# Kernel tuning notes

Measured on AMD Instinct MI355X. Metric: run time of the kernel, lower is better.

## Reference

```python
import jax, jax.numpy as jnp
import numpy as np
from jax import lax

B = 16384
NWIRES = 4


def _conv(x, w, b):
    # NCHW conv, stride 1, SAME padding (pad 1 for k=3)
    y = lax.conv_general_dilated(x, w, (1, 1), ((1, 1), (1, 1)),
                                 dimension_numbers=("NCHW", "OIHW", "NCHW"))
    return y + b[None, :, None, None]


def _pool2(x):
    b, c, h, w = x.shape
    return x.reshape(b, c, h // 2, 2, w // 2, 2).max(axis=(3, 5))


def _apply_1q(state, U, wire):
    # state: (B,2,2,2,2) complex; U: (B,2,2) complex
    s = jnp.moveaxis(state, wire + 1, -1)
    s = jnp.einsum("bij,b...j->b...i", U, s)
    return jnp.moveaxis(s, -1, wire + 1)


def _apply_cnot(state, c, t):
    s0 = jnp.take(state, 0, axis=c + 1)
    s1 = jnp.take(state, 1, axis=c + 1)
    ta = t + 1 if t < c else t  # target axis index after removing control axis
    s1 = jnp.flip(s1, axis=ta)
    return jnp.stack([s0, s1], axis=c + 1)


def _ry(th):
    c = jnp.cos(th / 2)
    s = jnp.sin(th / 2)
    U = jnp.stack([jnp.stack([c, -s], -1), jnp.stack([s, c], -1)], -2)
    return U.astype(jnp.complex64)


def _rz(th):
    e = jnp.exp(-0.5j * th.astype(jnp.complex64))
    z = jnp.zeros_like(e)
    return jnp.stack([jnp.stack([e, z], -1), jnp.stack([z, jnp.conj(e)], -1)], -2)


def _rx(th):
    c = jnp.cos(th / 2).astype(jnp.complex64)
    s = jnp.sin(th / 2).astype(jnp.complex64)
    return jnp.stack([jnp.stack([c, -1j * s], -1), jnp.stack([-1j * s, c], -1)], -2)


def _circuit(params):
    # params: (B, 16) -> PauliZ expvals (B, 4)
    b = params.shape[0]
    state = jnp.zeros((b, 16), jnp.complex64).at[:, 0].set(1.0).reshape(b, 2, 2, 2, 2)
    for i in range(NWIRES):
        state = _apply_1q(state, _ry(params[:, 4 * i + 0]), i)
        state = _apply_1q(state, _rz(params[:, 4 * i + 1]), i)
        state = _apply_1q(state, _rx(params[:, 4 * i + 2]), i)
        state = _apply_cnot(state, i, (i + 1) % NWIRES)
    probs = state.real ** 2 + state.imag ** 2  # (B,2,2,2,2)
    zs = []
    for i in range(NWIRES):
        p = probs.sum(axis=tuple(a for a in range(1, 5) if a != i + 1))  # (B,2)
        zs.append(p[:, 0] - p[:, 1])
    return jnp.stack(zs, axis=-1)


def setup_inputs() -> dict:
    key = jax.random.key(0)
    ks = jax.random.split(key, 12)
    d = {}
    d["x"] = jax.random.normal(ks[0], (B, 1, 28, 28), jnp.float32)
    d["conv1_w"] = jax.random.normal(ks[1], (4, 1, 3, 3), jnp.float32) * 0.3
    d["conv1_b"] = jax.random.normal(ks[2], (4,), jnp.float32) * 0.1
    d["conv2_w"] = jax.random.normal(ks[3], (4, 4, 3, 3), jnp.float32) * 0.15
    d["conv2_b"] = jax.random.normal(ks[4], (4,), jnp.float32) * 0.1
    d["pl_w"] = jax.random.normal(ks[5], (16, 196), jnp.float32) * 0.07
    d["pl_b"] = jax.random.normal(ks[6], (16,), jnp.float32) * 0.05
    d["ro_w"] = jax.random.normal(ks[7], (4, 4), jnp.float32) * 0.5
    d["ro_b"] = jax.random.normal(ks[8], (4,), jnp.float32) * 0.1
    d["bn_w"] = jnp.ones((4,), jnp.float32)
    d["bn_b"] = jnp.zeros((4,), jnp.float32)
    return d


def reference(x, conv1_w, conv1_b, conv2_w, conv2_b, pl_w, pl_b, ro_w, ro_b, bn_w, bn_b):
    h = _pool2(jax.nn.relu(_conv(x, conv1_w, conv1_b)))   # (B,4,14,14)
    h = _pool2(jax.nn.relu(_conv(h, conv2_w, conv2_b)))   # (B,4,7,7)
    flat = h.reshape(x.shape[0], -1)                      # (B,196)
    params = flat @ pl_w.T + pl_b                         # (B,16)
    z = _circuit(params)                                  # (B,4)
    out = z @ ro_w.T + ro_b                               # (B,4)
    mean = out.mean(0)
    var = out.var(0)  # biased, matches torch BN training normalization
    return (out - mean) / jnp.sqrt(var + 1e-5) * bn_w + bn_b
```

## Files before the change

### kernel.cpp

```cpp
#include <hip/hip_runtime.h>
#include <math.h>

#define BATCH 16384

typedef float v2f __attribute__((ext_vector_type(2)));
typedef unsigned short u16;
typedef __attribute__((ext_vector_type(8))) short short8;
typedef __attribute__((ext_vector_type(4))) float f32x4;

__device__ __forceinline__ v2f pk_fma(v2f a, v2f b, v2f c) {
  return __builtin_elementwise_fma(a, b, c);
}
__device__ __forceinline__ v2f pk_max(v2f a, v2f b) {
  return __builtin_elementwise_max(a, b);
}

__device__ __forceinline__ unsigned bf2(float lo, float hi) {
  unsigned a = __float_as_uint(lo);
  unsigned b = __float_as_uint(hi);
  a = (a + 0x7fffu + ((a >> 16) & 1u)) >> 16;
  b = (b + 0x7fffu + ((b >> 16) & 1u)) & 0xffff0000u;
  return a | b;
}

__device__ __forceinline__ unsigned cvtpk(float lo, float hi) {
  unsigned r;
  asm("v_cvt_pk_bf16_f32 %0, %1, %2" : "=v"(r) : "v"(lo), "v"(hi));
  return r;
}

__global__ __launch_bounds__(256) void qnat_fused(
    const float* __restrict__ x,
    const float* __restrict__ w1,
    const float* __restrict__ b1,
    const float* __restrict__ w2,
    const float* __restrict__ b2,
    const float* __restrict__ plw,
    const float* __restrict__ plb,
    const float* __restrict__ rw,
    const float* __restrict__ rb,
    float* __restrict__ pre,
    float* __restrict__ stats)
{
  __shared__ __align__(16) unsigned h1sh[16 * 513];
  __shared__ __align__(16) u16 h2b[16][232];
  __shared__ __align__(16) uint4 plw_tb[28 * 16];
  __shared__ __align__(16) u16 b2f[64 * 16];
  __shared__ float s_red[4][8];

  const int tid = threadIdx.x;
  const int w = tid >> 6;
  const int lane = tid & 63;
  const int base = (blockIdx.x * 4 + w) * 4;

  #pragma unroll
  for (int j = 0; j < 2; j++) {
    int s = tid + 256 * j;
    if (s < 448) {
      int tp = s >> 4;
      int k2 = s & 15;
      uint4 v = make_uint4(0u, 0u, 0u, 0u);
      if (tp < 25) {
        const float4* pr = (const float4*)(plw + k2 * 196);
        float4 a = pr[2 * tp];
        float4 b = (tp < 24) ? pr[2 * tp + 1] : make_float4(0.f, 0.f, 0.f, 0.f);
        v = make_uint4(bf2(a.x, a.y), bf2(a.z, a.w),
                       bf2(b.x, b.y), bf2(b.z, b.w));
      }
      plw_tb[s] = v;
    }
  }

  #pragma unroll
  for (int j = 0; j < 4; j++) {
    int e = tid + 256 * j;
    int kk = e >> 4, n = e & 15;
    int ci = kk >> 4, dy = (kk >> 2) & 3, dx = kk & 3;
    int co = n >> 2, sy = (n >> 1) & 1, sx = n & 1;
    int ry = dy - sy, rx = dx - sx;
    float v = 0.0f;
    if (ry >= 0 && ry < 3 && rx >= 0 && rx < 3)
      v = w2[((co * 4 + ci) * 3 + ry) * 3 + rx];
    b2f[e] = (u16)bf2(v, 0.0f);
  }

  {
    uint4 z4 = make_uint4(0u, 0u, 0u, 0u);
    uint4* hz = (uint4*)h1sh;
    #pragma unroll
    for (int t = 0; t < 9; t++) {
      int p = tid + 256 * t;
      if (p < 2052) hz[p] = z4;
    }
    uint4* hz2 = (uint4*)h2b;
    #pragma unroll
    for (int t = 0; t < 2; t++) {
      int p = tid + 256 * t;
      if (p < 464) hz2[p] = z4;
    }
  }
  __syncthreads();

  const int i = lane >> 2;
  const int q = lane & 3;
  const bool c1act = lane < 56;

  float4 pfa[4], pfb[4];
  float pe0[4], pe1[4];
  #pragma unroll
  for (int r = 0; r < 4; r++) {
    pfa[r] = make_float4(0,0,0,0); pfb[r] = make_float4(0,0,0,0);
    pe0[r] = 0.0f; pe1[r] = 0.0f;
  }

  if (c1act) {
    const float* xb = x + (size_t)base * 784;
    #pragma unroll
    for (int r = 0; r < 4; r++) {
      int row = 2 * i - 1 + r;
      if (0 <= row && row < 28) {
        const float* rp = xb + row * 28;
        pfa[r] = *(const float4*)(rp + 8 * q);
        if (q > 0) pe0[r] = rp[8 * q - 1];
        if (q < 3) {
          pfb[r] = *(const float4*)(rp + 8 * q + 4);
          pe1[r] = rp[8 * q + 8];
        }
      }
    }
  }

  #pragma unroll 1
  for (int it = 0; it < 4; ++it) {
    if (c1act) {
      float win[4][10];
      #pragma unroll
      for (int r = 0; r < 4; r++) {
        win[r][0] = pe0[r];
        win[r][1] = pfa[r].x; win[r][2] = pfa[r].y;
        win[r][3] = pfa[r].z; win[r][4] = pfa[r].w;
        win[r][5] = pfb[r].x; win[r][6] = pfb[r].y;
        win[r][7] = pfb[r].z; win[r][8] = pfb[r].w;
        win[r][9] = pe1[r];
      }
      if (it != 3) {
        const float* xn = x + (size_t)(base + it + 1) * 784;
        #pragma unroll
        for (int r = 0; r < 4; r++) {
          int row = 2 * i - 1 + r;
          pfa[r] = make_float4(0,0,0,0);
          pfb[r] = make_float4(0,0,0,0);
          pe0[r] = 0.0f; pe1[r] = 0.0f;
          if (0 <= row && row < 28) {
            const float* rp = xn + row * 28;
            pfa[r] = *(const float4*)(rp + 8 * q);
            if (q > 0) pe0[r] = rp[8 * q - 1];
            if (q < 3) {
              pfb[r] = *(const float4*)(rp + 8 * q + 4);
              pe1[r] = rp[8 * q + 8];
            }
          }
        }
      }
      v2f P[4][9];
      #pragma unroll
      for (int r = 0; r < 4; r++)
        #pragma unroll
        for (int k = 0; k < 9; k++) P[r][k] = (v2f){win[r][k], win[r][k + 1]};

      u16* hs = (u16*)h1sh + (4 * w + it) * 1026 + (i + 1) * 16 + 4 * q;
      #pragma unroll
      for (int c = 0; c < 4; c++) {
        const float* wc = w1 + c * 9;
        const v2f bias2 = (v2f){b1[c], b1[c]};
        v2f a0[4], a1[4];
        #pragma unroll
        for (int jj = 0; jj < 4; jj++) { a0[jj] = bias2; a1[jj] = bias2; }
        #pragma unroll
        for (int dy = 0; dy < 3; dy++)
          #pragma unroll
          for (int dx = 0; dx < 3; dx++) {
            const float wv = wc[dy * 3 + dx];
            const v2f wvv = (v2f){wv, wv};
            #pragma unroll
            for (int jj = 0; jj < 4; jj++) {
              a0[jj] = pk_fma(P[dy][2 * jj + dx],     wvv, a0[jj]);
              a1[jj] = pk_fma(P[dy + 1][2 * jj + dx], wvv, a1[jj]);
            }
          }
        float m[4];
        #pragma unroll
        for (int jj = 0; jj < 4; jj++) {
          v2f mm = pk_max(a0[jj], a1[jj]);
          m[jj] = fmaxf(fmaxf(mm.x, mm.y), 0.0f);
        }
        u16* p = hs + c * 256;
        p[1] = (u16)cvtpk(m[0], m[0]);
        if (q < 3) {
          *(unsigned*)(p + 2) = cvtpk(m[1], m[2]);
          p[4] = (u16)cvtpk(m[3], m[3]);
        } else {
          p[2] = (u16)cvtpk(m[1], m[1]);
        }
      }
    }
  }
  __syncthreads();

  {
    const int n = lane & 15;
    const int g = lane >> 4;
    short8 bfr0, bfr1;
    #pragma unroll
    for (int j = 0; j < 8; j++) {
      bfr0[j] = (short)b2f[(8 * g + j) * 16 + n];
      bfr1[j] = (short)b2f[(32 + 8 * g + j) * 16 + n];
    }
    const float b2v = b2[n >> 2];
    const int ci0 = g >> 1;
    const int dy0 = 2 * (g & 1);
    const int dbase = n * 513 + ci0 * 128 + dy0 * 8;
    const unsigned* hp = h1sh;

    #pragma unroll 2
    for (int t = 0; t < 13; t++) {
      int p = 4 * t + w;
      if (p < 49) {
        int i2 = (p * 9363) >> 16;
        int j2 = p - 7 * i2;
        int d = dbase + i2 * 16 + j2;
        f32x4 acc = {0.f, 0.f, 0.f, 0.f};
        {
          unsigned A0 = hp[d],       A1 = hp[d + 1];
          unsigned A2 = hp[d + 8],   A3 = hp[d + 9];
          short8 av = __builtin_bit_cast(short8, make_uint4(A0, A1, A2, A3));
          acc = __builtin_amdgcn_mfma_f32_16x16x32_bf16(av, bfr0, acc, 0, 0, 0);
        }
        {
          unsigned A0 = hp[d + 256], A1 = hp[d + 257];
          unsigned A2 = hp[d + 264], A3 = hp[d + 265];
          short8 av = __builtin_bit_cast(short8, make_uint4(A0, A1, A2, A3));
          acc = __builtin_amdgcn_mfma_f32_16x16x32_bf16(av, bfr1, acc, 0, 0, 0);
        }
        float r0 = acc[0], r1 = acc[1], r2 = acc[2], r3 = acc[3];
        r0 = fmaxf(r0, __shfl_xor(r0, 1, 64)); r0 = fmaxf(r0, __shfl_xor(r0, 2, 64));
        r1 = fmaxf(r1, __shfl_xor(r1, 1, 64)); r1 = fmaxf(r1, __shfl_xor(r1, 2, 64));
        r2 = fmaxf(r2, __shfl_xor(r2, 1, 64)); r2 = fmaxf(r2, __shfl_xor(r2, 2, 64));
        r3 = fmaxf(r3, __shfl_xor(r3, 1, 64)); r3 = fmaxf(r3, __shfl_xor(r3, 2, 64));
        if ((lane & 3) == 0) {
          int co = n >> 2;
          u16* hq = &h2b[4 * g][49 * co + p];
          float v0 = fmaxf(r0 + b2v, 0.0f);
          float v1 = fmaxf(r1 + b2v, 0.0f);
          float v2 = fmaxf(r2 + b2v, 0.0f);
          float v3 = fmaxf(r3 + b2v, 0.0f);
          hq[0]       = (u16)cvtpk(v0, v0);
          hq[232]     = (u16)cvtpk(v1, v1);
          hq[464]     = (u16)cvtpk(v2, v2);
          hq[696]     = (u16)cvtpk(v3, v3);
        }
      }
    }
  }
  __syncthreads();

  const int s2 = lane >> 4;
  const int k = lane & 15;

  float cv, sv;
  {
    const int arow = lane & 15;
    const int kg = lane >> 4;
    const short8* ha = (const short8*)&h2b[arow][0];
    const short8* hbw = (const short8*)plw_tb;
    f32x4 acc = {0.f, 0.f, 0.f, 0.f};
    #pragma unroll
    for (int kt = 0; kt < 7; kt++) {
      short8 av = ha[4 * kt + kg];
      short8 bv = hbw[(4 * kt + kg) * 16 + arow];
      acc = __builtin_amdgcn_mfma_f32_16x16x32_bf16(av, bv, acc, 0, 0, 0);
    }
    const int srcl = 16 * w + k;
    float c0 = __shfl(acc[0], srcl, 64);
    float c1 = __shfl(acc[1], srcl, 64);
    float c2 = __shfl(acc[2], srcl, 64);
    float c3 = __shfl(acc[3], srcl, 64);
    float pv = (s2 & 2) ? ((s2 & 1) ? c3 : c2) : ((s2 & 1) ? c1 : c0);
    pv += plb[k];
    __sincosf(pv * 0.5f, &sv, &cv);
  }

  {
    const int l = k;
    const int gb = lane & 48;
    float re = (l == 0) ? 1.0f : 0.0f;
    float im = 0.0f;
    #pragma unroll
    for (int qi = 0; qi < 4; qi++) {
      const int beta = 3 - qi;
      const int m = 1 << beta;
      const int b = (l >> beta) & 1;
      float c = __shfl(cv, gb + 4 * qi, 64), s = __shfl(sv, gb + 4 * qi, 64);
      float pr_ = __shfl_xor(re, m, 64), pi_ = __shfl_xor(im, m, 64);
      float sg = b ? s : -s;
      re = fmaf(c, re, sg * pr_);
      im = fmaf(c, im, sg * pi_);
      c = __shfl(cv, gb + 4 * qi + 1, 64); s = __shfl(sv, gb + 4 * qi + 1, 64);
      float sz = b ? s : -s;
      float nr = c * re - sz * im;
      float ni = c * im + sz * re;
      re = nr; im = ni;
      c = __shfl(cv, gb + 4 * qi + 2, 64); s = __shfl(sv, gb + 4 * qi + 2, 64);
      pr_ = __shfl_xor(re, m, 64); pi_ = __shfl_xor(im, m, 64);
      nr = fmaf(c, re, s * pi_);
      ni = fmaf(c, im, -s * pr_);
      re = nr; im = ni;
      const int tm = 1 << (3 - ((qi + 1) & 3));
      float fr = __shfl_xor(re, tm, 64), fi = __shfl_xor(im, tm, 64);
      if (b) { re = fr; im = fi; }
    }
    float pr2 = re * re + im * im;
    float z0 = ((l >> 3) & 1) ? -pr2 : pr2;
    float z1 = ((l >> 2) & 1) ? -pr2 : pr2;
    float z2 = ((l >> 1) & 1) ? -pr2 : pr2;
    float z3 = (l & 1) ? -pr2 : pr2;
    #pragma unroll
    for (int off = 8; off >= 1; off >>= 1) {
      z0 += __shfl_xor(z0, off, 64);
      z1 += __shfl_xor(z1, off, 64);
      z2 += __shfl_xor(z2, off, 64);
      z3 += __shfl_xor(z3, off, 64);
    }
    float as0 = 0.f, as1 = 0.f, as2 = 0.f, as3 = 0.f;
    float aq0 = 0.f, aq1 = 0.f, aq2 = 0.f, aq3 = 0.f;
    if (l == 0) {
      float o0 = fmaf(rw[0],  z0, fmaf(rw[1],  z1, fmaf(rw[2],  z2, fmaf(rw[3],  z3, rb[0]))));
      float o1 = fmaf(rw[4],  z0, fmaf(rw[5],  z1, fmaf(rw[6],  z2, fmaf(rw[7],  z3, rb[1]))));
      float o2 = fmaf(rw[8],  z0, fmaf(rw[9],  z1, fmaf(rw[10], z2, fmaf(rw[11], z3, rb[2]))));
      float o3 = fmaf(rw[12], z0, fmaf(rw[13], z1, fmaf(rw[14], z2, fmaf(rw[15], z3, rb[3]))));
      *(float4*)(pre + (size_t)(base + s2) * 4) = make_float4(o0, o1, o2, o3);
      as0 = o0; aq0 = o0 * o0;
      as1 = o1; aq1 = o1 * o1;
      as2 = o2; aq2 = o2 * o2;
      as3 = o3; aq3 = o3 * o3;
    }
    #pragma unroll
    for (int off = 32; off >= 16; off >>= 1) {
      as0 += __shfl_down(as0, off, 64); aq0 += __shfl_down(aq0, off, 64);
      as1 += __shfl_down(as1, off, 64); aq1 += __shfl_down(aq1, off, 64);
      as2 += __shfl_down(as2, off, 64); aq2 += __shfl_down(aq2, off, 64);
      as3 += __shfl_down(as3, off, 64); aq3 += __shfl_down(aq3, off, 64);
    }
    if (lane == 0) {
      s_red[w][0] = as0; s_red[w][4] = aq0;
      s_red[w][1] = as1; s_red[w][5] = aq1;
      s_red[w][2] = as2; s_red[w][6] = aq2;
      s_red[w][3] = as3; s_red[w][7] = aq3;
    }
  }
  __syncthreads();
  if (tid < 8) {
    float v = s_red[0][tid] + s_red[1][tid] + s_red[2][tid] + s_red[3][tid];
    atomicAdd(&stats[tid], v);
  }
}

__global__ __launch_bounds__(256) void qnat_bn(
    float* __restrict__ pre,
    const float* __restrict__ stats,
    const float* __restrict__ bnw,
    const float* __restrict__ bnb)
{
  int idx = blockIdx.x * 256 + threadIdx.x;
  int c = idx & 3;
  float mean = stats[c] * (1.0f / BATCH);
  float ex2 = stats[4 + c] * (1.0f / BATCH);
  float var = ex2 - mean * mean;
  float inv = rsqrtf(var + 1e-5f);
  pre[idx] = (pre[idx] - mean) * inv * bnw[c] + bnb[c];
}

extern "C" void kernel_launch(void* const* d_in, const int* in_sizes, int n_in,
                              void* d_out, int out_size, void* d_ws, size_t ws_size,
                              hipStream_t stream) {
  const float* x   = (const float*)d_in[0];
  const float* w1  = (const float*)d_in[1];
  const float* b1  = (const float*)d_in[2];
  const float* w2  = (const float*)d_in[3];
  const float* b2  = (const float*)d_in[4];
  const float* plw = (const float*)d_in[5];
  const float* plb = (const float*)d_in[6];
  const float* rw  = (const float*)d_in[7];
  const float* rb  = (const float*)d_in[8];
  const float* bnw = (const float*)d_in[9];
  const float* bnb = (const float*)d_in[10];

  float* out   = (float*)d_out;
  float* stats = (float*)d_ws;

  hipMemsetAsync(stats, 0, 8 * sizeof(float), stream);
  qnat_fused<<<BATCH / 16, 256, 0, stream>>>(x, w1, b1, w2, b2, plw, plb, rw, rb, out, stats);
  qnat_bn<<<(BATCH * 4) / 256, 256, 0, stream>>>(out, stats, bnw, bnb);
}
```

Before: 130.1 us.

## Interleave conv1 and conv2 per sample iteration with small shared buffer

Shrinks the conv1 output buffer from all 16 samples to one sample per warp, and runs the conv2 MFMA stage inside the per-sample loop with a block barrier after each iteration. It also pre-packs the conv2 B fragments as short8 in shared memory and folds the bias into the accumulator init. The aim is a much smaller LDS footprint for higher occupancy and vectorized B-fragment loads. The cost is extra __syncthreads per iteration and a different MFMA row mapping across samples.

```diff
diff --git a/kernel.cpp b/kernel.cpp
--- a/kernel.cpp
+++ b/kernel.cpp
@@ -42,10 +42,10 @@
     float* __restrict__ pre,
     float* __restrict__ stats)
 {
-  __shared__ __align__(16) unsigned h1sh[16 * 513];
+  __shared__ __align__(16) unsigned h1cur[4][513];
   __shared__ __align__(16) u16 h2b[16][232];
   __shared__ __align__(16) uint4 plw_tb[28 * 16];
-  __shared__ __align__(16) u16 b2f[64 * 16];
+  __shared__ __align__(16) short8 b2ft[128];
   __shared__ float s_red[4][8];
 
   const int tid = threadIdx.x;
@@ -71,26 +71,30 @@
     }
   }
 
-  #pragma unroll
-  for (int j = 0; j < 4; j++) {
-    int e = tid + 256 * j;
-    int kk = e >> 4, n = e & 15;
-    int ci = kk >> 4, dy = (kk >> 2) & 3, dx = kk & 3;
+  if (tid < 128) {
+    int h = tid >> 6, g = (tid >> 4) & 3, n = tid & 15;
     int co = n >> 2, sy = (n >> 1) & 1, sx = n & 1;
-    int ry = dy - sy, rx = dx - sx;
-    float v = 0.0f;
-    if (ry >= 0 && ry < 3 && rx >= 0 && rx < 3)
-      v = w2[((co * 4 + ci) * 3 + ry) * 3 + rx];
-    b2f[e] = (u16)bf2(v, 0.0f);
+    short8 bv;
+    #pragma unroll
+    for (int j = 0; j < 8; j++) {
+      int s = 32 * h + 8 * g + j;
+      int ci = s >> 4, dy = (s >> 2) & 3, dx = s & 3;
+      int ry = dy - sy, rx = dx - sx;
+      float v = 0.0f;
+      if (ry >= 0 && ry < 3 && rx >= 0 && rx < 3)
+        v = w2[((co * 4 + ci) * 3 + ry) * 3 + rx];
+      bv[j] = (short)(u16)bf2(v, 0.0f);
+    }
+    b2ft[tid] = bv;
   }
 
   {
     uint4 z4 = make_uint4(0u, 0u, 0u, 0u);
-    uint4* hz = (uint4*)h1sh;
-    #pragma unroll
-    for (int t = 0; t < 9; t++) {
+    uint4* hz = (uint4*)h1cur;
+    #pragma unroll
+    for (int t = 0; t < 3; t++) {
       int p = tid + 256 * t;
-      if (p < 2052) hz[p] = z4;
+      if (p < 513) hz[p] = z4;
     }
     uint4* hz2 = (uint4*)h2b;
     #pragma unroll
@@ -168,7 +172,7 @@
         #pragma unroll
         for (int k = 0; k < 9; k++) P[r][k] = (v2f){win[r][k], win[r][k + 1]};
 
-      u16* hs = (u16*)h1sh + (4 * w + it) * 1026 + (i + 1) * 16 + 4 * q;
+      u16* hs = (u16*)&h1cur[w][0] + (i + 1) * 16 + 4 * q;
       #pragma unroll
       for (int c = 0; c < 4; c++) {
         const float* wc = w1 + c * 9;
@@ -204,65 +208,55 @@
         }
       }
     }
-  }
-  __syncthreads();
-
-  {
-    const int n = lane & 15;
-    const int g = lane >> 4;
-    short8 bfr0, bfr1;
-    #pragma unroll
-    for (int j = 0; j < 8; j++) {
-      bfr0[j] = (short)b2f[(8 * g + j) * 16 + n];
-      bfr1[j] = (short)b2f[(32 + 8 * g + j) * 16 + n];
-    }
-    const float b2v = b2[n >> 2];
-    const int ci0 = g >> 1;
-    const int dy0 = 2 * (g & 1);
-    const int dbase = n * 513 + ci0 * 128 + dy0 * 8;
-    const unsigned* hp = h1sh;
-
-    #pragma unroll 2
-    for (int t = 0; t < 13; t++) {
-      int p = 4 * t + w;
-      if (p < 49) {
+    __syncthreads();
+
+    {
+      const int n2 = lane & 15;
+      const int g2 = lane >> 4;
+      short8 bfr0 = b2ft[g2 * 16 + n2];
+      short8 bfr1 = b2ft[64 + g2 * 16 + n2];
+      const float bias = b2[n2 >> 2];
+      const int msA = lane & 3;
+      const int psA = (lane >> 2) & 3;
+      const int ciA = g2 >> 1;
+      const int dy0 = 2 * (g2 & 1);
+      const unsigned* h1 = &h1cur[0][0];
+
+      for (int G = w; G < 13; G += 4) {
+        int p = 4 * G + psA;
         int i2 = (p * 9363) >> 16;
         int j2 = p - 7 * i2;
-        int d = dbase + i2 * 16 + j2;
-        f32x4 acc = {0.f, 0.f, 0.f, 0.f};
-        {
-          unsigned A0 = hp[d],       A1 = hp[d + 1];
-          unsigned A2 = hp[d + 8],   A3 = hp[d + 9];
-          short8 av = __builtin_bit_cast(short8, make_uint4(A0, A1, A2, A3));
-          acc = __builtin_amdgcn_mfma_f32_16x16x32_bf16(av, bfr0, acc, 0, 0, 0);
-        }
-        {
-          unsigned A0 = hp[d + 256], A1 = hp[d + 257];
-          unsigned A2 = hp[d + 264], A3 = hp[d + 265];
-          short8 av = __builtin_bit_cast(short8, make_uint4(A0, A1, A2, A3));
-          acc = __builtin_amdgcn_mfma_f32_16x16x32_bf16(av, bfr1, acc, 0, 0, 0);
-        }
+        int a = msA * 513 + ciA * 128 + (2 * i2 + dy0) * 8 + j2;
+        unsigned A0 = h1[a],       A1 = h1[a + 1];
+        unsigned A2 = h1[a + 8],   A3 = h1[a + 9];
+        short8 av0 = __builtin_bit_cast(short8, make_uint4(A0, A1, A2, A3));
+        unsigned B0 = h1[a + 256], B1 = h1[a + 257];
+        unsigned B2 = h1[a + 264], B3 = h1[a + 265];
+        short8 av1 = __builtin_bit_cast(short8, make_uint4(B0, B1, B2, B3));
+        f32x4 acc = {bias, bias, bias, bias};
+        acc = __builtin_amdgcn_mfma_f32_16x16x32_bf16(av0, bfr0, acc, 0, 0, 0);
+        acc = __builtin_amdgcn_mfma_f32_16x16x32_bf16(av1, bfr1, acc, 0, 0, 0);
         float r0 = acc[0], r1 = acc[1], r2 = acc[2], r3 = acc[3];
         r0 = fmaxf(r0, __shfl_xor(r0, 1, 64)); r0 = fmaxf(r0, __shfl_xor(r0, 2, 64));
         r1 = fmaxf(r1, __shfl_xor(r1, 1, 64)); r1 = fmaxf(r1, __shfl_xor(r1, 2, 64));
         r2 = fmaxf(r2, __shfl_xor(r2, 1, 64)); r2 = fmaxf(r2, __shfl_xor(r2, 2, 64));
         r3 = fmaxf(r3, __shfl_xor(r3, 1, 64)); r3 = fmaxf(r3, __shfl_xor(r3, 2, 64));
-        if ((lane & 3) == 0) {
-          int co = n >> 2;
-          u16* hq = &h2b[4 * g][49 * co + p];
-          float v0 = fmaxf(r0 + b2v, 0.0f);
-          float v1 = fmaxf(r1 + b2v, 0.0f);
-          float v2 = fmaxf(r2 + b2v, 0.0f);
-          float v3 = fmaxf(r3 + b2v, 0.0f);
-          hq[0]       = (u16)cvtpk(v0, v0);
-          hq[232]     = (u16)cvtpk(v1, v1);
-          hq[464]     = (u16)cvtpk(v2, v2);
-          hq[696]     = (u16)cvtpk(v3, v3);
-        }
-      }
-    }
-  }
-  __syncthreads();
+        int pst = 4 * G + g2;
+        if ((lane & 3) == 0 && pst < 49) {
+          int off = 49 * (n2 >> 2) + pst;
+          float v0 = fmaxf(r0, 0.0f);
+          float v1 = fmaxf(r1, 0.0f);
+          float v2 = fmaxf(r2, 0.0f);
+          float v3 = fmaxf(r3, 0.0f);
+          h2b[it][off]      = (u16)cvtpk(v0, v0);
+          h2b[4 + it][off]  = (u16)cvtpk(v1, v1);
+          h2b[8 + it][off]  = (u16)cvtpk(v2, v2);
+          h2b[12 + it][off] = (u16)cvtpk(v3, v3);
+        }
+      }
+    }
+    __syncthreads();
+  }
 
   const int s2 = lane >> 4;
   const int k = lane & 15;
```

Result: slower. 133.3 us (+2.4%).
